# Optimization experiments

Hardware: AMD Instinct MI355X
Metric: run time of the kernel (lower is better)

Reference implementation:

```python
import jax, jax.numpy as jnp
import numpy as np

NUM_HEADS = 12


def setup_inputs() -> dict:
    key = jax.random.key(0)
    ks = jax.random.split(key, 6)
    B, T, D = 512, 128, 768  # batch, seq (<= CONTEXT_LENGTH=128), d_model
    d_in, d_out = D, D
    s_in = 1.0 / np.sqrt(d_in)
    s_out = 1.0 / np.sqrt(d_out)
    return {
        "x": jax.random.normal(ks[0], (B, T, d_in), dtype=jnp.float32),
        "Wq": jax.random.uniform(ks[1], (d_in, d_out), jnp.float32, -s_in, s_in),
        "Wk": jax.random.uniform(ks[2], (d_in, d_out), jnp.float32, -s_in, s_in),
        "Wv": jax.random.uniform(ks[3], (d_in, d_out), jnp.float32, -s_in, s_in),
        "Wo": jax.random.uniform(ks[4], (d_out, d_out), jnp.float32, -s_out, s_out),
        "bo": jax.random.uniform(ks[5], (d_out,), jnp.float32, -s_out, s_out),
    }


def reference(x, Wq, Wk, Wv, Wo, bo):
    B, T, _ = x.shape
    H = NUM_HEADS
    hd = Wq.shape[1] // H
    # projections -> [b, h, t, hd]
    q = jnp.einsum("btd,de->bte", x, Wq).reshape(B, T, H, hd).transpose(0, 2, 1, 3)
    k = jnp.einsum("btd,de->bte", x, Wk).reshape(B, T, H, hd).transpose(0, 2, 1, 3)
    v = jnp.einsum("btd,de->bte", x, Wv).reshape(B, T, H, hd).transpose(0, 2, 1, 3)
    scores = jnp.einsum("bhqd,bhkd->bhqk", q, k)
    causal = jnp.tril(jnp.ones((T, T), dtype=bool))  # True = keep
    scores = jnp.where(causal, scores, -jnp.inf)
    attn = jax.nn.softmax(scores / jnp.sqrt(jnp.float32(hd)), axis=-1)
    # dropout is identity in eval mode
    ctx = jnp.einsum("bhqk,bhkd->bhqd", attn, v)
    ctx = ctx.transpose(0, 2, 1, 3).reshape(B, T, H * hd)
    return jnp.einsum("btd,de->bte", ctx, Wo) + bo
```

## Files before the change

kernel.cpp:

```cpp
#include <hip/hip_runtime.h>
#include <hip/hip_bf16.h>
#include <cstdint>
#include <math.h>


typedef __bf16 bf16;
typedef __bf16 bf16x8 __attribute__((ext_vector_type(8)));
typedef float f32x4 __attribute__((ext_vector_type(4)));

#define MFMA16(a, b, c) __builtin_amdgcn_mfma_f32_16x16x32_bf16((a), (b), (c), 0, 0, 0)

#define GLD_LDS16(gp, lp)                                                       \
  __builtin_amdgcn_global_load_lds(                                             \
      (const __attribute__((address_space(1))) void*)(gp),                      \
      (__attribute__((address_space(3))) void*)(lp), 16, 0, 0)

__global__ __launch_bounds__(256) void cast_x_bf16(const float* __restrict__ in,
                                                   bf16* __restrict__ out, int n) {
  int i = (blockIdx.x * 256 + threadIdx.x) * 4;
  if (i < n) {
    float4 v = *(const float4*)(in + i);
    bf16 o[4] = {(bf16)v.x, (bf16)v.y, (bf16)v.z, (bf16)v.w};
    *(uint2*)(out + i) = *(const uint2*)o;
  }
}

__global__ __launch_bounds__(256) void transpose_cast_w(const float* __restrict__ W,
                                                        bf16* __restrict__ Out) {
  __shared__ float t[32][33];
  int bx = blockIdx.x * 32;
  int by = blockIdx.y * 32;
  int tx = threadIdx.x, ty = threadIdx.y;
  for (int i = 0; i < 32; i += 8)
    t[ty + i][tx] = W[(size_t)(bx + ty + i) * 768 + by + tx];
  __syncthreads();
  for (int i = 0; i < 32; i += 8)
    Out[(size_t)(by + ty + i) * 768 + bx + tx] = (bf16)t[tx][ty + i];
}

template <bool OUT_F32>
__global__ __launch_bounds__(256) void gemm128(const bf16* __restrict__ A, int lda,
                                               const bf16* __restrict__ Bt, int ldb,
                                               void* __restrict__ Cout, int ldc,
                                               const float* __restrict__ bias, int K) {
  __shared__ bf16 sA[128 * 32];
  __shared__ bf16 sB[128 * 32];
  const int tid = threadIdx.x;
  const int lane = tid & 63;
  const int w = tid >> 6;
  const int wm = (w & 1) * 64;
  const int wn = (w >> 1) * 64;
  const int m0 = blockIdx.x * 128;
  const int n0 = blockIdx.y * 128;

  f32x4 acc[4][4];
  for (int i = 0; i < 4; ++i)
    for (int j = 0; j < 4; ++j) acc[i][j] = (f32x4){0.f, 0.f, 0.f, 0.f};

  const int lm = lane & 15;
  const int kq = (lane >> 4) * 8;

  for (int k0 = 0; k0 < K; k0 += 32) {
    for (int i = 0; i < 2; ++i) {
      int chunk = w * 2 + i;
      int e = chunk * 512 + lane * 8;
      int r = e >> 5;
      int c = e & 31;
      GLD_LDS16(A + (size_t)(m0 + r) * lda + k0 + c, sA + chunk * 512);
      GLD_LDS16(Bt + (size_t)(n0 + r) * ldb + k0 + c, sB + chunk * 512);
    }
    __syncthreads();

    bf16x8 af[4], bfr[4];
    for (int mi = 0; mi < 4; ++mi)
      af[mi] = *(const bf16x8*)(sA + (wm + mi * 16 + lm) * 32 + kq);
    for (int ni = 0; ni < 4; ++ni)
      bfr[ni] = *(const bf16x8*)(sB + (wn + ni * 16 + lm) * 32 + kq);
    for (int mi = 0; mi < 4; ++mi)
      for (int ni = 0; ni < 4; ++ni)
        acc[mi][ni] = MFMA16(af[mi], bfr[ni], acc[mi][ni]);
    __syncthreads();
  }

  const int lr = (lane >> 4) * 4;
  for (int mi = 0; mi < 4; ++mi)
    for (int ni = 0; ni < 4; ++ni) {
      int col = n0 + wn + ni * 16 + lm;
      for (int r = 0; r < 4; ++r) {
        int row = m0 + wm + mi * 16 + lr + r;
        float v = acc[mi][ni][r];
        if (OUT_F32)
          ((float*)Cout)[(size_t)row * ldc + col] = v + bias[col];
        else
          ((bf16*)Cout)[(size_t)row * ldc + col] = (bf16)v;
      }
    }
}

__global__ __launch_bounds__(256) void attn_kernel(const bf16* __restrict__ qkv,
                                                   bf16* __restrict__ ctx) {
  constexpr int LDQ = 2304;
  constexpr int SQS = 72;
  constexpr int SPS = 136;
  __shared__ bf16 smem[27136];
  bf16* sQ = smem;
  bf16* sK = smem + 128 * SQS;
  bf16* sVt = smem + 2 * 128 * SQS;
  bf16* sP = smem;

  const int bh = blockIdx.x;
  const int b = bh / 12, h = bh % 12;
  const bf16* Qg = qkv + (size_t)b * 128 * LDQ + h * 64;
  const bf16* Kg = Qg + 768;
  const bf16* Vg = Qg + 1536;

  const int tid = threadIdx.x;
  {
    int row = tid >> 1, half = tid & 1;
    const uint4* qsrc = (const uint4*)(Qg + (size_t)row * LDQ + half * 32);
    const uint4* ksrc = (const uint4*)(Kg + (size_t)row * LDQ + half * 32);
    const uint4* vsrc = (const uint4*)(Vg + (size_t)row * LDQ + half * 32);
    uint4* qdst = (uint4*)(sQ + row * SQS + half * 32);
    uint4* kdst = (uint4*)(sK + row * SQS + half * 32);
    uint4 vt[4];
    for (int i = 0; i < 4; ++i) {
      qdst[i] = qsrc[i];
      kdst[i] = ksrc[i];
      vt[i] = vsrc[i];
    }
    const bf16* tp = (const bf16*)vt;
    for (int d = 0; d < 32; ++d) sVt[(half * 32 + d) * SPS + row] = tp[d];
  }
  __syncthreads();

  const int lane = tid & 63;
  const int w = tid >> 6;
  const int lm = lane & 15;
  const int kq = (lane >> 4) * 8;
  const int lr = (lane >> 4) * 4;

  f32x4 sacc[2][8];
  for (int i = 0; i < 2; ++i)
    for (int j = 0; j < 8; ++j) sacc[i][j] = (f32x4){0.f, 0.f, 0.f, 0.f};
  for (int kk = 0; kk < 64; kk += 32) {
    bf16x8 aq[2], bk[8];
    for (int mi = 0; mi < 2; ++mi)
      aq[mi] = *(const bf16x8*)(sQ + (w * 32 + mi * 16 + lm) * SQS + kk + kq);
    for (int ni = 0; ni < 8; ++ni)
      bk[ni] = *(const bf16x8*)(sK + (ni * 16 + lm) * SQS + kk + kq);
    for (int mi = 0; mi < 2; ++mi)
      for (int ni = 0; ni < 8; ++ni)
        sacc[mi][ni] = MFMA16(aq[mi], bk[ni], sacc[mi][ni]);
  }

  float inv[2][4];
  for (int mi = 0; mi < 2; ++mi) {
    for (int r = 0; r < 4; ++r) {
      int row = w * 32 + mi * 16 + lr + r;
      float vals[8];
      float mx = -INFINITY;
      for (int ni = 0; ni < 8; ++ni) {
        int col = ni * 16 + lm;
        float v = sacc[mi][ni][r] * 0.125f;
        if (col > row) v = -INFINITY;
        vals[ni] = v;
        mx = fmaxf(mx, v);
      }
      for (int off = 1; off < 16; off <<= 1) mx = fmaxf(mx, __shfl_xor(mx, off, 64));
      float sum = 0.f;
      for (int ni = 0; ni < 8; ++ni) {
        float p = __expf(vals[ni] - mx);
        vals[ni] = p;
        sum += p;
      }
      for (int off = 1; off < 16; off <<= 1) sum += __shfl_xor(sum, off, 64);
      inv[mi][r] = 1.f / sum;
      for (int ni = 0; ni < 8; ++ni) sacc[mi][ni][r] = vals[ni];
    }
  }
  __syncthreads();

  for (int mi = 0; mi < 2; ++mi)
    for (int ni = 0; ni < 8; ++ni)
      for (int r = 0; r < 4; ++r) {
        int row = w * 32 + mi * 16 + lr + r;
        int col = ni * 16 + lm;
        sP[row * SPS + col] = (bf16)sacc[mi][ni][r];
      }
  __syncthreads();

  f32x4 oacc[2][4];
  for (int i = 0; i < 2; ++i)
    for (int j = 0; j < 4; ++j) oacc[i][j] = (f32x4){0.f, 0.f, 0.f, 0.f};
  for (int kk = 0; kk < 128; kk += 32) {
    bf16x8 ap[2], bv[4];
    for (int mi = 0; mi < 2; ++mi)
      ap[mi] = *(const bf16x8*)(sP + (w * 32 + mi * 16 + lm) * SPS + kk + kq);
    for (int ci = 0; ci < 4; ++ci)
      bv[ci] = *(const bf16x8*)(sVt + (ci * 16 + lm) * SPS + kk + kq);
    for (int mi = 0; mi < 2; ++mi)
      for (int ci = 0; ci < 4; ++ci)
        oacc[mi][ci] = MFMA16(ap[mi], bv[ci], oacc[mi][ci]);
  }

  bf16* Cg = ctx + (size_t)b * 128 * LDQ + h * 64;
  for (int mi = 0; mi < 2; ++mi)
    for (int ci = 0; ci < 4; ++ci)
      for (int r = 0; r < 4; ++r) {
        int row = w * 32 + mi * 16 + lr + r;
        int col = ci * 16 + lm;
        Cg[(size_t)row * LDQ + col] = (bf16)(oacc[mi][ci][r] * inv[mi][r]);
      }
}

extern "C" void kernel_launch(void* const* d_in, const int* in_sizes, int n_in,
                              void* d_out, int out_size, void* d_ws, size_t ws_size,
                              hipStream_t stream) {
  const float* x = (const float*)d_in[0];
  const float* Wq = (const float*)d_in[1];
  const float* Wk = (const float*)d_in[2];
  const float* Wv = (const float*)d_in[3];
  const float* Wo = (const float*)d_in[4];
  const float* bo = (const float*)d_in[5];
  float* out = (float*)d_out;

  constexpr int M = 512 * 128;
  constexpr int D = 768;
  constexpr size_t XB_BYTES = (size_t)M * D * 2;
  constexpr size_t WQKV_BYTES = (size_t)3 * D * D * 2;
  constexpr size_t WOT_BYTES = (size_t)D * D * 2;

  char* ws = (char*)d_ws;
  bf16* xb = (bf16*)ws;
  bf16* wqkv = (bf16*)(ws + XB_BYTES);
  bf16* wot = (bf16*)(ws + XB_BYTES + WQKV_BYTES);
  bf16* qkv = (bf16*)(ws + XB_BYTES + WQKV_BYTES + WOT_BYTES);

  cast_x_bf16<<<(M * D) / 1024, 256, 0, stream>>>(x, xb, M * D);
  dim3 tb(32, 8);
  transpose_cast_w<<<dim3(24, 24), tb, 0, stream>>>(Wq, wqkv);
  transpose_cast_w<<<dim3(24, 24), tb, 0, stream>>>(Wk, wqkv + 768 * 768);
  transpose_cast_w<<<dim3(24, 24), tb, 0, stream>>>(Wv, wqkv + 2 * 768 * 768);
  transpose_cast_w<<<dim3(24, 24), tb, 0, stream>>>(Wo, wot);
  gemm128<false><<<dim3(M / 128, 2304 / 128), 256, 0, stream>>>(
      xb, 768, wqkv, 768, qkv, 2304, nullptr, 768);
  attn_kernel<<<512 * 12, 256, 0, stream>>>(qkv, qkv);
  gemm128<true><<<dim3(M / 128, 768 / 128), 256, 0, stream>>>(
      qkv, 2304, wot, 768, out, 768, bo, 768);
}
```

Before: 899.4 us.

## Rewrite GEMM as 256x256-tile, 4-stage pipelined kernel with swizzled LDS

Replaces the 128x128 single-buffered GEMM with a 512-thread 256x256 tile kernel. It uses a 4-deep ring of LDS buffers filled by direct global-to-LDS loads, with explicit vmcnt waits so loads overlap MFMA work. An XOR swizzle on LDS columns targets bank conflicts, a workgroup remap groups tiles for cache locality, and setprio raises priority during the MFMA burst. Per-wave register accumulators double in size and 128KB of LDS is used per block, which limits occupancy.

```diff
diff --git a/kernel.cpp b/kernel.cpp
--- a/kernel.cpp
+++ b/kernel.cpp
@@ -39,60 +39,100 @@
 }
 
 template <bool OUT_F32>
-__global__ __launch_bounds__(256) void gemm128(const bf16* __restrict__ A, int lda,
-                                               const bf16* __restrict__ Bt, int ldb,
-                                               void* __restrict__ Cout, int ldc,
-                                               const float* __restrict__ bias, int K) {
-  __shared__ bf16 sA[128 * 32];
-  __shared__ bf16 sB[128 * 32];
+__global__ __launch_bounds__(512, 2) void gemm256(
+    const bf16* __restrict__ A, int lda, const bf16* __restrict__ Bt, int ldb,
+    void* __restrict__ Cout, int ldc, const float* __restrict__ bias, int K,
+    int ntn) {
+  __shared__ bf16 smem[4 * 16384];
+
   const int tid = threadIdx.x;
   const int lane = tid & 63;
   const int w = tid >> 6;
-  const int wm = (w & 1) * 64;
+
+  const int nwg = gridDim.x;
+  const int wg = (blockIdx.x & 7) * (nwg >> 3) + (blockIdx.x >> 3);
+  const int m0 = (wg / ntn) * 256;
+  const int n0 = (wg % ntn) * 256;
+
+  const int r0 = tid >> 2;
+  const int c0 = ((((tid & 3) * 16) ^ (((tid >> 3) & 3) << 4)) >> 1);
+  const bf16* Ablk = A + (size_t)m0 * lda;
+  const bf16* Bblk = Bt + (size_t)n0 * ldb;
+
+  const int lm = lane & 15;
+  const int kqs = ((lane >> 4) * 8) ^ (((lm >> 1) & 3) << 3);
+  const int wm = (w & 1) * 128;
   const int wn = (w >> 1) * 64;
-  const int m0 = blockIdx.x * 128;
-  const int n0 = blockIdx.y * 128;
-
-  f32x4 acc[4][4];
-  for (int i = 0; i < 4; ++i)
+
+  f32x4 acc[8][4];
+#pragma unroll
+  for (int i = 0; i < 8; ++i)
+#pragma unroll
     for (int j = 0; j < 4; ++j) acc[i][j] = (f32x4){0.f, 0.f, 0.f, 0.f};
 
-  const int lm = lane & 15;
-  const int kq = (lane >> 4) * 8;
-
-  for (int k0 = 0; k0 < K; k0 += 32) {
-    for (int i = 0; i < 2; ++i) {
-      int chunk = w * 2 + i;
-      int e = chunk * 512 + lane * 8;
-      int r = e >> 5;
-      int c = e & 31;
-      GLD_LDS16(A + (size_t)(m0 + r) * lda + k0 + c, sA + chunk * 512);
-      GLD_LDS16(Bt + (size_t)(n0 + r) * ldb + k0 + c, sB + chunk * 512);
-    }
-    __syncthreads();
-
-    bf16x8 af[4], bfr[4];
-    for (int mi = 0; mi < 4; ++mi)
-      af[mi] = *(const bf16x8*)(sA + (wm + mi * 16 + lm) * 32 + kq);
+  const int NT = K >> 5;
+
+#define STAGE(t)                                                                  \
+  {                                                                               \
+    bf16* sb = smem + ((t) & 3) * 16384;                                          \
+    const int k0 = (t) * 32;                                                      \
+    GLD_LDS16(Ablk + (size_t)r0 * lda + k0 + c0, sb + w * 512);                   \
+    GLD_LDS16(Ablk + (size_t)(128 + r0) * lda + k0 + c0, sb + 4096 + w * 512);    \
+    GLD_LDS16(Bblk + (size_t)r0 * ldb + k0 + c0, sb + 8192 + w * 512);            \
+    GLD_LDS16(Bblk + (size_t)(128 + r0) * ldb + k0 + c0, sb + 12288 + w * 512);   \
+  }
+
+  STAGE(0);
+  STAGE(1);
+  STAGE(2);
+  asm volatile("s_waitcnt vmcnt(8)" ::: "memory");
+  __builtin_amdgcn_s_barrier();
+  __builtin_amdgcn_sched_barrier(0);
+
+  for (int t = 0; t < NT; ++t) {
+    if (t + 3 < NT) STAGE(t + 3);
+
+    const bf16* base = smem + (t & 3) * 16384;
+    bf16x8 af[8], bfr[4];
+#pragma unroll
+    for (int mi = 0; mi < 8; ++mi)
+      af[mi] = *(const bf16x8*)(base + (wm + mi * 16 + lm) * 32 + kqs);
+#pragma unroll
     for (int ni = 0; ni < 4; ++ni)
-      bfr[ni] = *(const bf16x8*)(sB + (wn + ni * 16 + lm) * 32 + kq);
-    for (int mi = 0; mi < 4; ++mi)
+      bfr[ni] = *(const bf16x8*)(base + 8192 + (wn + ni * 16 + lm) * 32 + kqs);
+
+    __builtin_amdgcn_s_setprio(1);
+#pragma unroll
+    for (int mi = 0; mi < 8; ++mi)
+#pragma unroll
       for (int ni = 0; ni < 4; ++ni)
         acc[mi][ni] = MFMA16(af[mi], bfr[ni], acc[mi][ni]);
-    __syncthreads();
-  }
+    __builtin_amdgcn_s_setprio(0);
+
+    if (t + 3 < NT)
+      asm volatile("s_waitcnt vmcnt(8)" ::: "memory");
+    else if (t + 3 == NT)
+      asm volatile("s_waitcnt vmcnt(4)" ::: "memory");
+    else
+      asm volatile("s_waitcnt vmcnt(0)" ::: "memory");
+    __builtin_amdgcn_s_barrier();
+    __builtin_amdgcn_sched_barrier(0);
+  }
+#undef STAGE
 
   const int lr = (lane >> 4) * 4;
-  for (int mi = 0; mi < 4; ++mi)
+#pragma unroll
+  for (int mi = 0; mi < 8; ++mi)
+#pragma unroll
     for (int ni = 0; ni < 4; ++ni) {
-      int col = n0 + wn + ni * 16 + lm;
+      const int col = n0 + wn + ni * 16 + lm;
+#pragma unroll
       for (int r = 0; r < 4; ++r) {
-        int row = m0 + wm + mi * 16 + lr + r;
-        float v = acc[mi][ni][r];
-        if (OUT_F32)
-          ((float*)Cout)[(size_t)row * ldc + col] = v + bias[col];
+        const int row = m0 + wm + mi * 16 + lr + r;
+        if constexpr (OUT_F32)
+          ((float*)Cout)[(size_t)row * ldc + col] = acc[mi][ni][r] + bias[col];
         else
-          ((bf16*)Cout)[(size_t)row * ldc + col] = (bf16)v;
+          ((bf16*)Cout)[(size_t)row * ldc + col] = (bf16)acc[mi][ni][r];
       }
     }
 }
@@ -242,9 +282,9 @@
   transpose_cast_w<<<dim3(24, 24), tb, 0, stream>>>(Wk, wqkv + 768 * 768);
   transpose_cast_w<<<dim3(24, 24), tb, 0, stream>>>(Wv, wqkv + 2 * 768 * 768);
   transpose_cast_w<<<dim3(24, 24), tb, 0, stream>>>(Wo, wot);
-  gemm128<false><<<dim3(M / 128, 2304 / 128), 256, 0, stream>>>(
-      xb, 768, wqkv, 768, qkv, 2304, nullptr, 768);
+  gemm256<false><<<dim3(2304), 512, 0, stream>>>(xb, 768, wqkv, 768, qkv, 2304,
+                                                 nullptr, 768, 9);
   attn_kernel<<<512 * 12, 256, 0, stream>>>(qkv, qkv);
-  gemm128<true><<<dim3(M / 128, 768 / 128), 256, 0, stream>>>(
-      qkv, 2304, wot, 768, out, 768, bo, 768);
-}
+  gemm256<true><<<dim3(768), 512, 0, stream>>>(qkv, 2304, wot, 768, out, 768,
+                                               bo, 768, 3);
+}
```

Result: faster. 795.3 us (-11.6%).
